# Kernel tuning notes

Hardware: AMD Instinct MI355X
Metric: run time of the kernel (lower is better)

The kernel has to match this reference:

```python
import jax, jax.numpy as jnp
import numpy as np

N_NODES = 10000
N_EDGES = 320000
D = 256
L = 3
BN_EPS = 1e-5


def _segment_softmax(logits, seg, num_segments):
    # numerically stable softmax over variable-sized segments (incoming edges per node)
    m = jax.ops.segment_max(logits, seg, num_segments=num_segments)
    e = jnp.exp(logits - m[seg])
    s = jax.ops.segment_sum(e, seg, num_segments=num_segments)
    return e / s[seg]


def setup_inputs() -> dict:
    key = jax.random.key(0)
    ks = jax.random.split(key, 20)
    scale = 1.0 / np.sqrt(D)
    inp = {
        "x": jax.random.normal(ks[0], (N_NODES, D), dtype=jnp.float32),
        "edge_index": jax.random.randint(ks[1], (2, N_EDGES), 0, N_NODES, dtype=jnp.int64),
        # TransformerConv params (heads=1, concat=False)
        "Wq": jax.random.normal(ks[2], (D, D), jnp.float32) * scale,
        "bq": jnp.zeros((D,), jnp.float32),
        "Wk": jax.random.normal(ks[3], (D, D), jnp.float32) * scale,
        "bk": jnp.zeros((D,), jnp.float32),
        "Wv": jax.random.normal(ks[4], (D, D), jnp.float32) * scale,
        "bv": jnp.zeros((D,), jnp.float32),
        "Ws": jax.random.normal(ks[5], (D, D), jnp.float32) * scale,  # lin_skip (root weight)
        "bs": jnp.zeros((D,), jnp.float32),
        # SAGEConv params per layer: lin_l (neighbors, with bias), lin_r (root, no bias)
        "Wl": jax.random.normal(ks[6], (L, D, D), jnp.float32) * scale,
        "bl": jnp.zeros((L, D), jnp.float32),
        "Wr": jax.random.normal(ks[7], (L, D, D), jnp.float32) * scale,
        # BatchNorm affine params (eval mode: running_mean=0, running_var=1)
        "gamma": jnp.ones((L, D), jnp.float32) + 0.1 * jax.random.normal(ks[8], (L, D), jnp.float32),
        "beta": 0.1 * jax.random.normal(ks[9], (L, D), jnp.float32),
        # residual gate parameter (scalar)
        "alpha_res": jnp.asarray(0.5, jnp.float32),
    }
    return inp


def reference(x, edge_index, Wq, bq, Wk, bk, Wv, bv, Ws, bs, Wl, bl, Wr, gamma, beta, alpha_res):
    src, dst = edge_index[0], edge_index[1]  # message j -> i
    n, d = x.shape

    # ---- TransformerConv (heads=1, concat=False, eval: no dropout) ----
    q = x @ Wq + bq
    k = x @ Wk + bk
    v = x @ Wv + bv
    logits = jnp.sum(q[dst] * k[src], axis=-1) / jnp.sqrt(jnp.asarray(d, x.dtype))  # [E]
    attn = _segment_softmax(logits, dst, n)  # [E]
    agg = jax.ops.segment_sum(attn[:, None] * v[src], dst, num_segments=n)  # [N,D]
    h = agg + x @ Ws + bs  # root/skip connection
    h = jax.nn.relu(h)

    # in-degree for SAGE mean aggregation
    deg = jax.ops.segment_sum(jnp.ones((src.shape[0],), x.dtype), dst, num_segments=n)
    deg = jnp.maximum(deg, 1.0)[:, None]

    prev = h
    bn_scale = 1.0 / jnp.sqrt(1.0 + BN_EPS)  # eval-mode BN with running stats (0, 1)
    al = jax.nn.sigmoid(alpha_res)
    for i in range(Wl.shape[0]):
        mean_nb = jax.ops.segment_sum(h[src], dst, num_segments=n) / deg  # gather-mean-scatter
        z = mean_nb @ Wl[i] + bl[i] + h @ Wr[i]
        z = z * bn_scale * gamma[i] + beta[i]
        z = al * z + (1.0 - al) * prev
        h = jax.nn.relu(z)
        prev = h
    return h
```

## Files before the change

kernel.cpp:

```cpp
#include <hip/hip_runtime.h>
#include <hip/hip_bf16.h>

typedef unsigned short u16;
typedef unsigned int u32;
typedef unsigned char u8;
typedef __bf16 bf16x8 __attribute__((ext_vector_type(8)));
typedef float f32x4 __attribute__((ext_vector_type(4)));
typedef float f32x2 __attribute__((ext_vector_type(2)));

#define DIM 256
#define BN_SCALE 0.9999950000374997f

__device__ __forceinline__ float bf2f(u16 u) {
    union { unsigned u; float f; } c; c.u = ((unsigned)u) << 16; return c.f;
}
__device__ __forceinline__ u16 f2bf(float f) {
    union { float f; unsigned u; } c; c.f = f;
    unsigned u = c.u;
    unsigned r = (u + 0x7FFFu + ((u >> 16) & 1u)) >> 16;
    return (u16)r;
}
__device__ __forceinline__ float asf(unsigned u) {
    union { unsigned u; float f; } c; c.u = u; return c.f;
}
__device__ __forceinline__ void cvt8(int4 v, float* f) {
    unsigned a0 = (unsigned)v.x, a1 = (unsigned)v.y, a2 = (unsigned)v.z, a3 = (unsigned)v.w;
    f[0] = asf(a0 << 16); f[1] = asf(a0 & 0xFFFF0000u);
    f[2] = asf(a1 << 16); f[3] = asf(a1 & 0xFFFF0000u);
    f[4] = asf(a2 << 16); f[5] = asf(a2 & 0xFFFF0000u);
    f[6] = asf(a3 << 16); f[7] = asf(a3 & 0xFFFF0000u);
}
__device__ __forceinline__ void dec4(unsigned u, float* f) {
    f32x2 lo = __builtin_amdgcn_cvt_pk_f32_fp8((int)u, false);
    f32x2 hi = __builtin_amdgcn_cvt_pk_f32_fp8((int)u, true);
    f[0] = lo.x; f[1] = lo.y; f[2] = hi.x; f[3] = hi.y;
}
__device__ __forceinline__ unsigned pack4(float a, float b, float c, float d) {
    int u = __builtin_amdgcn_cvt_pk_fp8_f32(a, b, 0, false);
    u = __builtin_amdgcn_cvt_pk_fp8_f32(c, d, u, true);
    return (unsigned)u;
}
__device__ __forceinline__ void gl_lds16(const u16* g, u16* l) {
    __builtin_amdgcn_global_load_lds(
        (__attribute__((address_space(1))) const u32*)(const void*)g,
        (__attribute__((address_space(3))) u32*)(void*)l, 16, 0, 0);
}

__global__ void k_detect(const u16* __restrict__ xu, const long long* __restrict__ e64,
                         int* __restrict__ flags) {
    int lane = threadIdx.x;
    int plausible = 0;
#pragma unroll
    for (int j = 0; j < 4; ++j) {
        u16 u = xu[lane * 4 + j];
        int ex = (u >> 7) & 0xFF;
        plausible += (u == 0 || (ex >= 115 && ex <= 131)) ? 1 : 0;
    }
#pragma unroll
    for (int o = 32; o; o >>= 1) plausible += __shfl_xor(plausible, o, 64);
    long long hi = e64[lane] >> 32;
    unsigned long long b = __ballot(hi == 0);
    if (lane == 0) {
        flags[0] = (plausible >= 200) ? 1 : 0;
        flags[1] = (b == ~0ULL) ? 1 : 0;
    }
}

struct CvtDesc {
    const void* src[15];
    int cum[16];
};
__global__ void k_convert(CvtDesc d, const int* __restrict__ flags,
                          u16* __restrict__ arena, int total) {
    int i = blockIdx.x * 256 + threadIdx.x;
    if (i >= total) return;
    int t = 0;
    while (i >= d.cum[t + 1]) ++t;
    int j = i - d.cum[t];
    u16 v;
    if (flags[0]) v = ((const u16*)d.src[t])[j];
    else          v = f2bf(((const float*)d.src[t])[j]);
    arena[i] = v;
}

struct TDesc { const u16* src[12]; u16* dst[12]; };
__global__ __launch_bounds__(256) void k_transpose(TDesc td) {
    __shared__ u16 t[64][72];
    int m = blockIdx.x >> 4, tl = blockIdx.x & 15;
    int tr = (tl >> 2) * 64, tc = (tl & 3) * 64;
    const u16* S = td.src[m];
    u16* D = td.dst[m];
    int r = threadIdx.x >> 2, cs = (threadIdx.x & 3) * 16;
    *(int4*)&t[r][cs]     = *(const int4*)&S[(tr + r) * 256 + tc + cs];
    *(int4*)&t[r][cs + 8] = *(const int4*)&S[(tr + r) * 256 + tc + cs + 8];
    __syncthreads();
    u16 tmp[16];
#pragma unroll
    for (int j = 0; j < 16; ++j) tmp[j] = t[cs + j][r];
    *(int4*)&D[(tc + r) * 256 + tr + cs]     = *(int4*)&tmp[0];
    *(int4*)&D[(tc + r) * 256 + tr + cs + 8] = *(int4*)&tmp[8];
}

__global__ void k_edges(const int* __restrict__ ei32, const int* __restrict__ flags,
                        int* __restrict__ srcN, int* __restrict__ dstN,
                        int* __restrict__ deg, int E) {
    int e = blockIdx.x * 256 + threadIdx.x;
    if (e >= E) return;
    const long long* ei64 = (const long long*)ei32;
    int w64 = flags[1];
    int s = w64 ? (int)ei64[e]     : ei32[e];
    int d = w64 ? (int)ei64[E + e] : ei32[E + e];
    srcN[e] = s; dstN[e] = d;
    atomicAdd(&deg[d], 1);
}

__global__ __launch_bounds__(1024) void k_scan(const int* __restrict__ deg,
                                               int* __restrict__ offs,
                                               int* __restrict__ cursor, int N, int E) {
    __shared__ int s[1024];
    int t = threadIdx.x;
    int P = (N + 1023) >> 10;
    int base = t * P;
    int run = 0;
    for (int j = 0; j < P; ++j) { int idx = base + j; if (idx < N) run += deg[idx]; }
    s[t] = run;
    __syncthreads();
    int total = run;
    for (int off = 1; off < 1024; off <<= 1) {
        int v = 0;
        if (t >= off) v = s[t - off];
        __syncthreads();
        if (t >= off) s[t] += v;
        __syncthreads();
    }
    int r = s[t] - total;
    for (int j = 0; j < P; ++j) {
        int idx = base + j;
        if (idx < N) { offs[idx] = r; cursor[idx] = r; r += deg[idx]; }
    }
    if (t == 0) offs[N] = E;
}

__global__ void k_fill(const int* __restrict__ srcN, const int* __restrict__ dstN,
                       int* __restrict__ cursor, int* __restrict__ csr, int E) {
    int e = blockIdx.x * 256 + threadIdx.x;
    if (e < E) {
        int d = dstN[e];
        int pos = atomicAdd(&cursor[d], 1);
        csr[pos] = srcN[e];
    }
}

__global__ __launch_bounds__(256) void gemm_qkvs(
    const u16* __restrict__ x, const u16* __restrict__ WT,
    const u16* __restrict__ bias, u16* __restrict__ out, int M) {
    __shared__ __align__(16) u16 lds[16384];
    u16* As = lds;
    u16* Bs = lds + 8192;
    int tid = threadIdx.x, w = tid >> 6, lane = tid & 63;
    int l15 = lane & 15, quad = lane >> 4;
    int lr = lane >> 3, lc = lane & 7;
    int bm0 = blockIdx.x * 128, bn0 = blockIdx.y * 128;
    f32x4 acc[4][4];
#pragma unroll
    for (int a = 0; a < 4; ++a)
#pragma unroll
        for (int b = 0; b < 4; ++b) acc[a][b] = (f32x4){0.f, 0.f, 0.f, 0.f};

    for (int k0 = 0; k0 < 256; k0 += 64) {
#pragma unroll
        for (int j = 0; j < 4; ++j) {
            int ar = (w * 4 + j) * 8 + lr;
            int grow = bm0 + ar; if (grow >= M) grow = M - 1;
            gl_lds16(x + (size_t)grow * 256 + k0 + lc * 8, &As[(w * 4 + j) * 512]);
        }
#pragma unroll
        for (int j = 0; j < 4; ++j) {
            int nr = (w * 4 + j) * 8 + lr;
            gl_lds16(WT + (size_t)(bn0 + nr) * 256 + k0 + lc * 8, &Bs[(w * 4 + j) * 512]);
        }
        __syncthreads();
        int wm = w & 1, wn = w >> 1;
#pragma unroll
        for (int s = 0; s < 2; ++s) {
            bf16x8 a[4], b[4];
#pragma unroll
            for (int t = 0; t < 4; ++t)
                a[t] = *(const bf16x8*)&As[(wm * 64 + t * 16 + l15) * 64 + s * 32 + quad * 8];
#pragma unroll
            for (int t = 0; t < 4; ++t)
                b[t] = *(const bf16x8*)&Bs[(wn * 64 + t * 16 + l15) * 64 + s * 32 + quad * 8];
#pragma unroll
            for (int rt = 0; rt < 4; ++rt)
#pragma unroll
                for (int ct = 0; ct < 4; ++ct)
                    acc[rt][ct] = __builtin_amdgcn_mfma_f32_16x16x32_bf16(a[rt], b[ct], acc[rt][ct], 0, 0, 0);
        }
        __syncthreads();
    }
    int wm = w & 1, wn = w >> 1;
    u16* oL = lds + w * 4096;
#pragma unroll
    for (int rt = 0; rt < 4; ++rt)
#pragma unroll
        for (int ct = 0; ct < 4; ++ct) {
            int col = bn0 + wn * 64 + ct * 16 + l15;
            float bv = bf2f(bias[col]);
#pragma unroll
            for (int r = 0; r < 4; ++r)
                oL[(rt * 16 + quad * 4 + r) * 64 + ct * 16 + l15] = f2bf(acc[rt][ct][r] + bv);
        }
    __syncthreads();
#pragma unroll
    for (int j = 0; j < 8; ++j) {
        int orow = j * 8 + lr;
        int grow = bm0 + wm * 64 + orow;
        if (grow < M)
            *(int4*)&out[(size_t)grow * 1024 + bn0 + wn * 64 + lc * 8] = *(const int4*)&oL[orow * 64 + lc * 8];
    }
}

__global__ void k_pack8(const u16* __restrict__ qkvs, u8* __restrict__ kv8, int N) {
    int t = blockIdx.x * 256 + threadIdx.x;
    if (t >= N * 64) return;
    int i = t >> 6, s = t & 63;
    int4 v = *(const int4*)(qkvs + (size_t)i * 1024 + 256 + s * 8);
    float f[8]; cvt8(v, f);
    uint2 o;
    o.x = pack4(f[0], f[1], f[2], f[3]);
    o.y = pack4(f[4], f[5], f[6], f[7]);
    *(uint2*)(kv8 + (size_t)i * 512 + s * 8) = o;
}

__global__ __launch_bounds__(256) void k_attn(const u16* __restrict__ qkvs,
                                              const u8* __restrict__ kv8,
                                              const int* __restrict__ csr,
                                              const int* __restrict__ offs,
                                              u16* __restrict__ hb,
                                              u8* __restrict__ h8, int N) {
    int wv = threadIdx.x >> 6, lane = threadIdx.x & 63;
    int i = blockIdx.x * 4 + wv;
    if (i >= N) return;
    int sub = lane & 7;
    int e8 = lane >> 3;
    size_t row = (size_t)i * 1024;

    float qf[32];
    {
        const u16* qp = qkvs + row + sub * 32;
#pragma unroll
        for (int j = 0; j < 4; ++j) {
            int4 v = *(const int4*)(qp + j * 8);
            float t[8]; cvt8(v, t);
#pragma unroll
            for (int d = 0; d < 8; ++d) qf[j * 8 + d] = t[d] * 0.0625f;
        }
    }
    int e0 = offs[i], e1 = offs[i + 1];
    float m = -1e30f, denom = 0.f;
    float acc[32];
#pragma unroll
    for (int j = 0; j < 32; ++j) acc[j] = 0.f;

    for (int base = e0; base < e1; base += 8) {
        int e = base + e8;
        int sidx = csr[(e < e1) ? e : (e1 - 1)];
        const u8* kp = kv8 + (size_t)sidx * 512 + sub * 32;
        uint4 ka = *(const uint4*)kp;
        uint4 kb = *(const uint4*)(kp + 16);
        uint4 va = *(const uint4*)(kp + 256);
        uint4 vb = *(const uint4*)(kp + 272);
        unsigned kw[8] = {ka.x, ka.y, ka.z, ka.w, kb.x, kb.y, kb.z, kb.w};
        float p = 0.f;
#pragma unroll
        for (int j = 0; j < 8; ++j) {
            float t[4]; dec4(kw[j], t);
            p += qf[j * 4] * t[0] + qf[j * 4 + 1] * t[1] + qf[j * 4 + 2] * t[2] + qf[j * 4 + 3] * t[3];
        }
        p += __shfl_xor(p, 1, 64);
        p += __shfl_xor(p, 2, 64);
        p += __shfl_xor(p, 4, 64);
        if (e >= e1) p = -1e30f;
        float pm = p;
        pm = fmaxf(pm, __shfl_xor(pm, 8, 64));
        pm = fmaxf(pm, __shfl_xor(pm, 16, 64));
        pm = fmaxf(pm, __shfl_xor(pm, 32, 64));
        if (pm > m) {
            float sc = __expf(m - pm);
            denom *= sc;
#pragma unroll
            for (int j = 0; j < 32; ++j) acc[j] *= sc;
            m = pm;
        }
        float w = __expf(p - m);
        denom += w;
        unsigned vw[8] = {va.x, va.y, va.z, va.w, vb.x, vb.y, vb.z, vb.w};
#pragma unroll
        for (int j = 0; j < 8; ++j) {
            float t[4]; dec4(vw[j], t);
            acc[j * 4]     += w * t[0];
            acc[j * 4 + 1] += w * t[1];
            acc[j * 4 + 2] += w * t[2];
            acc[j * 4 + 3] += w * t[3];
        }
    }
    denom += __shfl_xor(denom, 8, 64);
    denom += __shfl_xor(denom, 16, 64);
    denom += __shfl_xor(denom, 32, 64);
    float inv = (denom > 0.f) ? 1.f / denom : 0.f;
#pragma unroll
    for (int j = 0; j < 32; ++j) {
        acc[j] += __shfl_xor(acc[j], 8, 64);
        acc[j] += __shfl_xor(acc[j], 16, 64);
        acc[j] += __shfl_xor(acc[j], 32, 64);
    }
    if (e8 == 0) {
        const u16* skp = qkvs + row + 768 + sub * 32;
        float h[32];
#pragma unroll
        for (int j = 0; j < 4; ++j) {
            int4 sv = *(const int4*)(skp + j * 8);
            float t[8]; cvt8(sv, t);
            u16 o[8];
#pragma unroll
            for (int d = 0; d < 8; ++d) {
                float hv = fmaxf(acc[j * 8 + d] * inv + t[d], 0.f);
                h[j * 8 + d] = hv;
                o[d] = f2bf(hv);
            }
            *(int4*)(hb + (size_t)i * 256 + sub * 32 + j * 8) = *(const int4*)o;
        }
        uint4 p0, p1;
        p0.x = pack4(h[0], h[1], h[2], h[3]);   p0.y = pack4(h[4], h[5], h[6], h[7]);
        p0.z = pack4(h[8], h[9], h[10], h[11]); p0.w = pack4(h[12], h[13], h[14], h[15]);
        p1.x = pack4(h[16], h[17], h[18], h[19]); p1.y = pack4(h[20], h[21], h[22], h[23]);
        p1.z = pack4(h[24], h[25], h[26], h[27]); p1.w = pack4(h[28], h[29], h[30], h[31]);
        *(uint4*)(h8 + (size_t)i * 256 + sub * 32) = p0;
        *(uint4*)(h8 + (size_t)i * 256 + sub * 32 + 16) = p1;
    }
}

__global__ __launch_bounds__(256) void k_agg(const u8* __restrict__ h8,
                                             const int* __restrict__ csr,
                                             const int* __restrict__ offs,
                                             u16* __restrict__ mean_out, int N) {
    int half = threadIdx.x >> 5, hl = threadIdx.x & 31;
    int i = blockIdx.x * 8 + half;
    if (i >= N) return;
    int e0 = offs[i], e1 = offs[i + 1];
    const u8* base = h8 + (unsigned)hl * 8;
    float acc[8];
#pragma unroll
    for (int d = 0; d < 8; ++d) acc[d] = 0.f;
    int e = e0;
    for (; e + 8 <= e1; e += 8) {
        uint2 r[8];
#pragma unroll
        for (int j = 0; j < 8; ++j)
            r[j] = *(const uint2*)(base + (size_t)csr[e + j] * 256);
#pragma unroll
        for (int j = 0; j < 8; ++j) {
            float f0[4], f1[4];
            dec4(r[j].x, f0); dec4(r[j].y, f1);
            acc[0] += f0[0]; acc[1] += f0[1]; acc[2] += f0[2]; acc[3] += f0[3];
            acc[4] += f1[0]; acc[5] += f1[1]; acc[6] += f1[2]; acc[7] += f1[3];
        }
    }
    for (; e < e1; ++e) {
        uint2 r0 = *(const uint2*)(base + (size_t)csr[e] * 256);
        float f0[4], f1[4];
        dec4(r0.x, f0); dec4(r0.y, f1);
        acc[0] += f0[0]; acc[1] += f0[1]; acc[2] += f0[2]; acc[3] += f0[3];
        acc[4] += f1[0]; acc[5] += f1[1]; acc[6] += f1[2]; acc[7] += f1[3];
    }
    int dg = e1 - e0; if (dg < 1) dg = 1;
    float inv = 1.f / (float)dg;
    u16 o16[8];
#pragma unroll
    for (int d = 0; d < 8; ++d) o16[d] = f2bf(acc[d] * inv);
    *(int4*)(mean_out + (size_t)i * 256 + (unsigned)hl * 8) = *(const int4*)o16;
}

__global__ __launch_bounds__(256) void gemm_sage(
    const u16* __restrict__ meanA, const u16* __restrict__ hin,
    const u16* __restrict__ WlT, const u16* __restrict__ WrT,
    const u16* __restrict__ bl, const u16* __restrict__ gamma,
    const u16* __restrict__ beta, const u16* __restrict__ alpha,
    u16* __restrict__ hout, u8* __restrict__ h8out, float* __restrict__ fout, int M) {
    __shared__ __align__(16) u16 lds[12288];
    u16* As = lds;
    u16* Bs = lds + 8192;
    int tid = threadIdx.x, w = tid >> 6, lane = tid & 63;
    int l15 = lane & 15, quad = lane >> 4;
    int lr = lane >> 3, lc = lane & 7;
    int bm0 = blockIdx.x * 128, n0 = blockIdx.y * 64;
    f32x4 acc[2][4];
#pragma unroll
    for (int a = 0; a < 2; ++a)
#pragma unroll
        for (int b = 0; b < 4; ++b) acc[a][b] = (f32x4){0.f, 0.f, 0.f, 0.f};

    for (int k0 = 0; k0 < 512; k0 += 64) {
        const u16* Asrc = (k0 < 256) ? meanA : hin;
        const u16* Bsrc = (k0 < 256) ? WlT : WrT;
        int kc = k0 & 255;
#pragma unroll
        for (int j = 0; j < 4; ++j) {
            int ar = (w * 4 + j) * 8 + lr;
            int grow = bm0 + ar; if (grow >= M) grow = M - 1;
            gl_lds16(Asrc + (size_t)grow * 256 + kc + lc * 8, &As[(w * 4 + j) * 512]);
        }
#pragma unroll
        for (int j = 0; j < 2; ++j) {
            int nr = (w * 2 + j) * 8 + lr;
            gl_lds16(Bsrc + (size_t)(n0 + nr) * 256 + kc + lc * 8, &Bs[(w * 2 + j) * 512]);
        }
        __syncthreads();
#pragma unroll
        for (int s = 0; s < 2; ++s) {
            bf16x8 a[2], b[4];
#pragma unroll
            for (int t = 0; t < 2; ++t)
                a[t] = *(const bf16x8*)&As[(w * 32 + t * 16 + l15) * 64 + s * 32 + quad * 8];
#pragma unroll
            for (int t = 0; t < 4; ++t)
                b[t] = *(const bf16x8*)&Bs[(t * 16 + l15) * 64 + s * 32 + quad * 8];
#pragma unroll
            for (int rt = 0; rt < 2; ++rt)
#pragma unroll
                for (int ct = 0; ct < 4; ++ct)
                    acc[rt][ct] = __builtin_amdgcn_mfma_f32_16x16x32_bf16(a[rt], b[ct], acc[rt][ct], 0, 0, 0);
        }
        __syncthreads();
    }

    float al = 1.f / (1.f + __expf(-bf2f(alpha[0])));
    float alc = 1.f - al;
    u16* oL = lds + w * 2048;
#pragma unroll
    for (int rt = 0; rt < 2; ++rt)
#pragma unroll
        for (int ct = 0; ct < 4; ++ct) {
            int col = n0 + ct * 16 + l15;
            float g  = bf2f(gamma[col]) * BN_SCALE;
            float be = bf2f(beta[col]);
            float bb = bf2f(bl[col]);
#pragma unroll
            for (int r = 0; r < 4; ++r) {
                int grow = bm0 + w * 32 + rt * 16 + quad * 4 + r;
                float z = (acc[rt][ct][r] + bb) * g + be;
                float prev = (grow < M) ? bf2f(hin[(size_t)grow * 256 + col]) : 0.f;
                z = al * z + alc * prev;
                z = fmaxf(z, 0.f);
                oL[(rt * 16 + quad * 4 + r) * 64 + ct * 16 + l15] = f2bf(z);
                if (fout && grow < M) fout[(size_t)grow * 256 + col] = z;
            }
        }
    __syncthreads();
#pragma unroll
    for (int j = 0; j < 4; ++j) {
        int orow = j * 8 + lr;
        int grow = bm0 + w * 32 + orow;
        if (grow < M) {
            int4 hv = *(const int4*)&oL[orow * 64 + lc * 8];
            *(int4*)&hout[(size_t)grow * 256 + n0 + lc * 8] = hv;
            float f[8]; cvt8(hv, f);
            uint2 o8;
            o8.x = pack4(f[0], f[1], f[2], f[3]);
            o8.y = pack4(f[4], f[5], f[6], f[7]);
            *(uint2*)(h8out + (size_t)grow * 256 + n0 + lc * 8) = o8;
        }
    }
}

extern "C" void kernel_launch(void* const* d_in, const int* in_sizes, int n_in,
                              void* d_out, int out_size, void* d_ws, size_t ws_size,
                              hipStream_t stream) {
    int N = in_sizes[0] / DIM;
    int E = in_sizes[1] / 2;
    int L = in_sizes[10] / (DIM * DIM);

    const int map[15] = {0, 2, 4, 6, 8, 10, 12, 3, 5, 7, 9, 11, 13, 14, 15};
    CvtDesc cd;
    cd.cum[0] = 0;
    for (int t = 0; t < 15; ++t) {
        cd.src[t] = d_in[map[t]];
        cd.cum[t + 1] = cd.cum[t] + in_sizes[map[t]];
    }
    int total = cd.cum[15];

    char* ws = (char*)d_ws;
    size_t off = 0;
    auto take = [&](size_t bytes) { size_t c = off; off = (off + bytes + 255) & ~255ULL; return c; };

    int* flags  = (int*)(ws + take(16));
    u16* arena  = (u16*)(ws + take((size_t)total * 2));
    u16* WT     = (u16*)(ws + take((size_t)(4 + 2 * L) * DIM * DIM * 2));
    int* srcN   = (int*)(ws + take((size_t)E * 4));
    int* dstN   = (int*)(ws + take((size_t)E * 4));
    int* csr    = (int*)(ws + take((size_t)E * 4));
    int* deg    = (int*)(ws + take((size_t)N * 4));
    int* offs   = (int*)(ws + take((size_t)(N + 1) * 4));
    int* cursor = (int*)(ws + take((size_t)N * 4));
    u16* hB0    = (u16*)(ws + take((size_t)N * DIM * 2));
    u8*  kv8    = (u8*)(ws + take((size_t)N * 512));
    u16* qkvsB  = (u16*)(ws + take((size_t)N * 1024 * 2));
    u16* meanB  = qkvsB;
    u16* hB1    = qkvsB + (size_t)N * DIM;
    u8*  h8     = (u8*)srcN;
    (void)ws_size; (void)n_in; (void)out_size;

    const u16* xb  = arena + cd.cum[0];
    const u16* Wqb = arena + cd.cum[1];
    const u16* Wkb = arena + cd.cum[2];
    const u16* Wvb = arena + cd.cum[3];
    const u16* Wsb = arena + cd.cum[4];
    const u16* Wlb = arena + cd.cum[5];
    const u16* Wrb = arena + cd.cum[6];
    const u16* biasF = arena + cd.cum[7];
    const u16* blb = arena + cd.cum[11];
    const u16* gmb = arena + cd.cum[12];
    const u16* btb = arena + cd.cum[13];
    const u16* alb = arena + cd.cum[14];

    k_detect<<<1, 64, 0, stream>>>((const u16*)d_in[0], (const long long*)d_in[1], flags);
    k_convert<<<(total + 255) / 256, 256, 0, stream>>>(cd, flags, arena, total);

    TDesc td;
    int nMat = 0;
    const u16* wsrc[4] = {Wqb, Wkb, Wvb, Wsb};
    for (int t = 0; t < 4; ++t) { td.src[nMat] = wsrc[t]; td.dst[nMat] = WT + (size_t)nMat * DIM * DIM; ++nMat; }
    for (int l = 0; l < L; ++l) { td.src[nMat] = Wlb + (size_t)l * DIM * DIM; td.dst[nMat] = WT + (size_t)nMat * DIM * DIM; ++nMat; }
    for (int l = 0; l < L; ++l) { td.src[nMat] = Wrb + (size_t)l * DIM * DIM; td.dst[nMat] = WT + (size_t)nMat * DIM * DIM; ++nMat; }
    k_transpose<<<nMat * 16, 256, 0, stream>>>(td);

    hipMemsetAsync(deg, 0, (size_t)N * 4, stream);
    int eb = (E + 255) / 256;
    k_edges<<<eb, 256, 0, stream>>>((const int*)d_in[1], flags, srcN, dstN, deg, E);
    k_scan<<<1, 1024, 0, stream>>>(deg, offs, cursor, N, E);
    k_fill<<<eb, 256, 0, stream>>>(srcN, dstN, cursor, csr, E);

    int Mb128 = (N + 127) / 128;
    gemm_qkvs<<<dim3(Mb128, 8), 256, 0, stream>>>(xb, WT, biasF, qkvsB, N);
    k_pack8<<<(N * 64 + 255) / 256, 256, 0, stream>>>(qkvsB, kv8, N);
    k_attn<<<(N + 3) / 4, 256, 0, stream>>>(qkvsB, kv8, csr, offs, hB0, h8, N);

    for (int l = 0; l < L; ++l) {
        const u16* hin = (l & 1) ? hB1 : hB0;
        u16* hout      = (l & 1) ? hB0 : hB1;
        float* fout = (l == L - 1) ? (float*)d_out : nullptr;
        k_agg<<<(N + 7) / 8, 256, 0, stream>>>(h8, csr, offs, meanB, N);
        gemm_sage<<<dim3(Mb128, 4), 256, 0, stream>>>(
            meanB, hin, WT + (size_t)(4 + l) * DIM * DIM, WT + (size_t)(4 + L + l) * DIM * DIM,
            blb + (size_t)l * DIM, gmb + (size_t)l * DIM, btb + (size_t)l * DIM,
            alb, hout, h8, fout, N);
    }
}
```

Baseline: 301.2 us.

## Fuse fp8 K/V packing into QKVS GEMM epilogue and split attention into two passes

The GEMM epilogue now writes fp8-packed K and V into separate arrays, which removes the standalone pack kernel and its extra read of the bf16 qkvs buffer. Attention is split into two kernels. The first computes and stores the per-edge logits along with the per-node max and inverse denominator. The second gathers only V and accumulates pre-normalised weights, so the online-softmax rescale of 32 accumulators is no longer needed. The cost is an extra kernel launch plus a write and re-read of E floats of logits, and each pass gathers a narrower per-neighbor row.

```diff
diff --git a/kernel.cpp b/kernel.cpp
--- a/kernel.cpp
+++ b/kernel.cpp
@@ -153,7 +153,8 @@
 
 __global__ __launch_bounds__(256) void gemm_qkvs(
     const u16* __restrict__ x, const u16* __restrict__ WT,
-    const u16* __restrict__ bias, u16* __restrict__ out, int M) {
+    const u16* __restrict__ bias, u16* __restrict__ out,
+    u8* __restrict__ k8, u8* __restrict__ v8, int M) {
     __shared__ __align__(16) u16 lds[16384];
     u16* As = lds;
     u16* Bs = lds + 8192;
@@ -211,43 +212,41 @@
                 oL[(rt * 16 + quad * 4 + r) * 64 + ct * 16 + l15] = f2bf(acc[rt][ct][r] + bv);
         }
     __syncthreads();
+    int c0 = bn0 + wn * 64 + lc * 8;
 #pragma unroll
     for (int j = 0; j < 8; ++j) {
         int orow = j * 8 + lr;
         int grow = bm0 + wm * 64 + orow;
-        if (grow < M)
-            *(int4*)&out[(size_t)grow * 1024 + bn0 + wn * 64 + lc * 8] = *(const int4*)&oL[orow * 64 + lc * 8];
-    }
-}
-
-__global__ void k_pack8(const u16* __restrict__ qkvs, u8* __restrict__ kv8, int N) {
-    int t = blockIdx.x * 256 + threadIdx.x;
-    if (t >= N * 64) return;
-    int i = t >> 6, s = t & 63;
-    int4 v = *(const int4*)(qkvs + (size_t)i * 1024 + 256 + s * 8);
-    float f[8]; cvt8(v, f);
-    uint2 o;
-    o.x = pack4(f[0], f[1], f[2], f[3]);
-    o.y = pack4(f[4], f[5], f[6], f[7]);
-    *(uint2*)(kv8 + (size_t)i * 512 + s * 8) = o;
-}
-
-__global__ __launch_bounds__(256) void k_attn(const u16* __restrict__ qkvs,
-                                              const u8* __restrict__ kv8,
-                                              const int* __restrict__ csr,
-                                              const int* __restrict__ offs,
-                                              u16* __restrict__ hb,
-                                              u8* __restrict__ h8, int N) {
+        if (grow < M) {
+            int4 hv = *(const int4*)&oL[orow * 64 + lc * 8];
+            *(int4*)&out[(size_t)grow * 1024 + c0] = hv;
+            if (c0 >= 256 && c0 < 768) {
+                float f[8]; cvt8(hv, f);
+                uint2 o8;
+                o8.x = pack4(f[0], f[1], f[2], f[3]);
+                o8.y = pack4(f[4], f[5], f[6], f[7]);
+                u8* dst = (c0 < 512) ? (k8 + (size_t)grow * 256 + (c0 - 256))
+                                     : (v8 + (size_t)grow * 256 + (c0 - 512));
+                *(uint2*)dst = o8;
+            }
+        }
+    }
+}
+
+__global__ __launch_bounds__(256) void k_attn1(const u16* __restrict__ qkvs,
+                                               const u8* __restrict__ k8,
+                                               const int* __restrict__ csr,
+                                               const int* __restrict__ offs,
+                                               float* __restrict__ le,
+                                               float2* __restrict__ md, int N) {
     int wv = threadIdx.x >> 6, lane = threadIdx.x & 63;
     int i = blockIdx.x * 4 + wv;
     if (i >= N) return;
-    int sub = lane & 7;
-    int e8 = lane >> 3;
-    size_t row = (size_t)i * 1024;
+    int sub = lane & 7, e8 = lane >> 3;
 
     float qf[32];
     {
-        const u16* qp = qkvs + row + sub * 32;
+        const u16* qp = qkvs + (size_t)i * 1024 + sub * 32;
 #pragma unroll
         for (int j = 0; j < 4; ++j) {
             int4 v = *(const int4*)(qp + j * 8);
@@ -258,18 +257,12 @@
     }
     int e0 = offs[i], e1 = offs[i + 1];
     float m = -1e30f, denom = 0.f;
-    float acc[32];
-#pragma unroll
-    for (int j = 0; j < 32; ++j) acc[j] = 0.f;
-
     for (int base = e0; base < e1; base += 8) {
         int e = base + e8;
         int sidx = csr[(e < e1) ? e : (e1 - 1)];
-        const u8* kp = kv8 + (size_t)sidx * 512 + sub * 32;
+        const u8* kp = k8 + (size_t)sidx * 256 + sub * 32;
         uint4 ka = *(const uint4*)kp;
         uint4 kb = *(const uint4*)(kp + 16);
-        uint4 va = *(const uint4*)(kp + 256);
-        uint4 vb = *(const uint4*)(kp + 272);
         unsigned kw[8] = {ka.x, ka.y, ka.z, ka.w, kb.x, kb.y, kb.z, kb.w};
         float p = 0.f;
 #pragma unroll
@@ -281,19 +274,54 @@
         p += __shfl_xor(p, 2, 64);
         p += __shfl_xor(p, 4, 64);
         if (e >= e1) p = -1e30f;
+        if (sub == 0 && e < e1) le[e] = p;
         float pm = p;
         pm = fmaxf(pm, __shfl_xor(pm, 8, 64));
         pm = fmaxf(pm, __shfl_xor(pm, 16, 64));
         pm = fmaxf(pm, __shfl_xor(pm, 32, 64));
         if (pm > m) {
-            float sc = __expf(m - pm);
-            denom *= sc;
-#pragma unroll
-            for (int j = 0; j < 32; ++j) acc[j] *= sc;
+            denom *= __expf(m - pm);
             m = pm;
         }
-        float w = __expf(p - m);
-        denom += w;
+        denom += __expf(p - m);
+    }
+    denom += __shfl_xor(denom, 8, 64);
+    denom += __shfl_xor(denom, 16, 64);
+    denom += __shfl_xor(denom, 32, 64);
+    if (lane == 0) {
+        float2 o; o.x = m; o.y = (denom > 0.f) ? 1.f / denom : 0.f;
+        md[i] = o;
+    }
+}
+
+__global__ __launch_bounds__(256) void k_attn2(const u16* __restrict__ qkvs,
+                                               const u8* __restrict__ v8,
+                                               const int* __restrict__ csr,
+                                               const int* __restrict__ offs,
+                                               const float* __restrict__ le,
+                                               const float2* __restrict__ md,
+                                               u16* __restrict__ hb,
+                                               u8* __restrict__ h8, int N) {
+    int wv = threadIdx.x >> 6, lane = threadIdx.x & 63;
+    int i = blockIdx.x * 4 + wv;
+    if (i >= N) return;
+    int sub = lane & 7, e8 = lane >> 3;
+    float2 c = md[i];
+    float m = c.x, invd = c.y;
+    int e0 = offs[i], e1 = offs[i + 1];
+    float acc[32];
+#pragma unroll
+    for (int j = 0; j < 32; ++j) acc[j] = 0.f;
+
+    for (int base = e0; base < e1; base += 8) {
+        int e = base + e8;
+        int eg = (e < e1) ? e : (e1 - 1);
+        int sidx = csr[eg];
+        float l = (e < e1) ? le[eg] : -1e30f;
+        const u8* vp = v8 + (size_t)sidx * 256 + sub * 32;
+        uint4 va = *(const uint4*)vp;
+        uint4 vb = *(const uint4*)(vp + 16);
+        float w = __expf(l - m) * invd;
         unsigned vw[8] = {va.x, va.y, va.z, va.w, vb.x, vb.y, vb.z, vb.w};
 #pragma unroll
         for (int j = 0; j < 8; ++j) {
@@ -304,10 +332,6 @@
             acc[j * 4 + 3] += w * t[3];
         }
     }
-    denom += __shfl_xor(denom, 8, 64);
-    denom += __shfl_xor(denom, 16, 64);
-    denom += __shfl_xor(denom, 32, 64);
-    float inv = (denom > 0.f) ? 1.f / denom : 0.f;
 #pragma unroll
     for (int j = 0; j < 32; ++j) {
         acc[j] += __shfl_xor(acc[j], 8, 64);
@@ -315,7 +339,7 @@
         acc[j] += __shfl_xor(acc[j], 32, 64);
     }
     if (e8 == 0) {
-        const u16* skp = qkvs + row + 768 + sub * 32;
+        const u16* skp = qkvs + (size_t)i * 1024 + 768 + sub * 32;
         float h[32];
 #pragma unroll
         for (int j = 0; j < 4; ++j) {
@@ -324,7 +348,7 @@
             u16 o[8];
 #pragma unroll
             for (int d = 0; d < 8; ++d) {
-                float hv = fmaxf(acc[j * 8 + d] * inv + t[d], 0.f);
+                float hv = fmaxf(acc[j * 8 + d] + t[d], 0.f);
                 h[j * 8 + d] = hv;
                 o[d] = f2bf(hv);
             }
@@ -503,7 +527,10 @@
     int* offs   = (int*)(ws + take((size_t)(N + 1) * 4));
     int* cursor = (int*)(ws + take((size_t)N * 4));
     u16* hB0    = (u16*)(ws + take((size_t)N * DIM * 2));
-    u8*  kv8    = (u8*)(ws + take((size_t)N * 512));
+    u8*  k8     = (u8*)(ws + take((size_t)N * 256));
+    u8*  v8     = (u8*)(ws + take((size_t)N * 256));
+    float* le   = (float*)(ws + take((size_t)E * 4));
+    float2* md  = (float2*)(ws + take((size_t)N * 8));
     u16* qkvsB  = (u16*)(ws + take((size_t)N * 1024 * 2));
     u16* meanB  = qkvsB;
     u16* hB1    = qkvsB + (size_t)N * DIM;
@@ -541,9 +568,9 @@
     k_fill<<<eb, 256, 0, stream>>>(srcN, dstN, cursor, csr, E);
 
     int Mb128 = (N + 127) / 128;
-    gemm_qkvs<<<dim3(Mb128, 8), 256, 0, stream>>>(xb, WT, biasF, qkvsB, N);
-    k_pack8<<<(N * 64 + 255) / 256, 256, 0, stream>>>(qkvsB, kv8, N);
-    k_attn<<<(N + 3) / 4, 256, 0, stream>>>(qkvsB, kv8, csr, offs, hB0, h8, N);
+    gemm_qkvs<<<dim3(Mb128, 8), 256, 0, stream>>>(xb, WT, biasF, qkvsB, k8, v8, N);
+    k_attn1<<<(N + 3) / 4, 256, 0, stream>>>(qkvsB, k8, csr, offs, le, md, N);
+    k_attn2<<<(N + 3) / 4, 256, 0, stream>>>(qkvsB, v8, csr, offs, le, md, hB0, h8, N);
 
     for (int l = 0; l < L; ++l) {
         const u16* hin = (l & 1) ? hB1 : hB0;
```

New measurement: 301.7 us. No clear change (+0.2%).
